# Optimization experiments

Hardware: AMD Instinct MI355X
Metric: run time of the kernel (lower is better)

Reference implementation:

```python
import jax, jax.numpy as jnp
import numpy as np

S = 80.0          # feature_size
LAMBDA_COORD = 5.0
LAMBDA_NOOBJ = 0.5


def setup_inputs() -> dict:
    key = jax.random.key(0)
    k1, k2, k3 = jax.random.split(key, 3)
    pred_tensor = jax.random.uniform(k1, (1024, 80, 80, 5), dtype=jnp.float32)
    target_boxes = jax.random.uniform(k2, (1024, 80, 80, 4), dtype=jnp.float32)
    obj_mask = jax.random.randint(k3, (1024, 80, 80), 0, 2, dtype=jnp.int32)
    return {"pred_tensor": pred_tensor, "target_boxes": target_boxes, "obj_mask": obj_mask}


def _xyxy(w, h):
    # Faithful to the original (buggy) conversion: pred_xyxy[:, :2] = pred[:, 2]/S - 0.5*pred[:, 2:4]
    # i.e. the 'center' used for BOTH x and y is w/S.
    c = w / S
    return c - 0.5 * w, c - 0.5 * h, c + 0.5 * w, c + 0.5 * h


def reference(pred_tensor, target_boxes, obj_mask):
    # pred_tensor: [N, 80, 80, 5]  (x, y, w, h, conf), target_boxes: [N, 80, 80, 4]
    m = (obj_mask > 0).astype(pred_tensor.dtype)        # coord_mask; (1-m) is noobj_mask
    px, py, pw, ph, pc = (pred_tensor[..., i] for i in range(5))
    tx, ty, tw, th = (target_boxes[..., i] for i in range(4))

    # per-cell 1x1 IoU (B=1, so the response-assignment loop is trivial: mask always 1)
    px1, py1, px2, py2 = _xyxy(pw, ph)
    tx1, ty1, tx2, ty2 = _xyxy(tw, th)
    iw = jnp.maximum(jnp.minimum(px2, tx2) - jnp.maximum(px1, tx1), 0.0)
    ih = jnp.maximum(jnp.minimum(py2, ty2) - jnp.maximum(py1, ty1), 0.0)
    inter = iw * ih
    union = pw * ph + tw * th - inter
    iou = jax.lax.stop_gradient(inter / union)          # original uses max_iou.data (detached)

    loss_xy = jnp.sum(m * ((px - tx) ** 2 + (py - ty) ** 2))
    loss_wh = jnp.sum(m * ((jnp.sqrt(pw) - jnp.sqrt(tw)) ** 2 + (jnp.sqrt(ph) - jnp.sqrt(th)) ** 2))
    loss_obj = jnp.sum(m * (pc - iou) ** 2)
    loss_noobj = jnp.sum((1.0 - m) * pc ** 2)           # noobj target conf is 0

    batch = pred_tensor.shape[0]
    loss = (LAMBDA_COORD * (loss_xy + loss_wh) + loss_obj + LAMBDA_NOOBJ * loss_noobj) / batch
    return loss
```

## Files before the change

### kernel.cpp

```cpp
#include <hip/hip_runtime.h>


#define S_INV (1.0f / 80.0f)

__global__ void zero_out_kernel(float* out) {
    out[0] = 0.0f;
}

__global__ __launch_bounds__(256) void yolo_loss_kernel(
    const float4* __restrict__ pred4,
    const float4* __restrict__ targ4,
    const int4*  __restrict__ mask4,
    float* __restrict__ out,
    int ngroups)
{
    __shared__ float4 lp[5 * 256];
    __shared__ float4 lt[5 * 256];

    const int t = threadIdx.x;
    float acc = 0.0f;

    for (int base = blockIdx.x * 256; base < ngroups; base += gridDim.x * 256) {
        #pragma unroll
        for (int i = 0; i < 5; ++i)
            lp[i * 256 + t] = pred4[base * 5 + i * 256 + t];
        #pragma unroll
        for (int i = 0; i < 4; ++i) {
            int j = i * 256 + t;
            lt[j + (j >> 2)] = targ4[base * 4 + j];
        }
        int4 mi = mask4[base + t];
        int mm[4] = { mi.x, mi.y, mi.z, mi.w };
        __syncthreads();

        float p[20];
        float tv[16];
        #pragma unroll
        for (int i = 0; i < 5; ++i) {
            float4 v = lp[5 * t + i];
            p[4 * i + 0] = v.x; p[4 * i + 1] = v.y; p[4 * i + 2] = v.z; p[4 * i + 3] = v.w;
        }
        #pragma unroll
        for (int i = 0; i < 4; ++i) {
            float4 v = lt[5 * t + i];
            tv[4 * i + 0] = v.x; tv[4 * i + 1] = v.y; tv[4 * i + 2] = v.z; tv[4 * i + 3] = v.w;
        }

        #pragma unroll
        for (int j = 0; j < 4; ++j) {
            float px = p[5 * j + 0], py = p[5 * j + 1], pw = p[5 * j + 2];
            float ph = p[5 * j + 3], pc = p[5 * j + 4];
            float tx = tv[4 * j + 0], ty = tv[4 * j + 1], tw = tv[4 * j + 2], th = tv[4 * j + 3];

            float cp = pw * S_INV;
            float ct = tw * S_INV;
            float px1 = cp - 0.5f * pw, py1 = cp - 0.5f * ph;
            float px2 = cp + 0.5f * pw, py2 = cp + 0.5f * ph;
            float tx1 = ct - 0.5f * tw, ty1 = ct - 0.5f * th;
            float tx2 = ct + 0.5f * tw, ty2 = ct + 0.5f * th;

            float iw = fmaxf(fminf(px2, tx2) - fmaxf(px1, tx1), 0.0f);
            float ih = fmaxf(fminf(py2, ty2) - fmaxf(py1, ty1), 0.0f);
            float inter = iw * ih;
            float uni = pw * ph + tw * th - inter;
            float iou = inter / uni;

            float dx = px - tx, dy = py - ty;
            float sw = sqrtf(pw) - sqrtf(tw);
            float sh = sqrtf(ph) - sqrtf(th);
            float dobj = pc - iou;

            float obj_term = 5.0f * ((dx * dx + dy * dy) + (sw * sw + sh * sh)) + dobj * dobj;
            float noobj_term = 0.5f * pc * pc;
            acc += (mm[j] > 0) ? obj_term : noobj_term;
        }
        __syncthreads();
    }

    #pragma unroll
    for (int off = 32; off > 0; off >>= 1)
        acc += __shfl_down(acc, off, 64);

    __shared__ float wsum[4];
    int lane = threadIdx.x & 63;
    int wid = threadIdx.x >> 6;
    if (lane == 0) wsum[wid] = acc;
    __syncthreads();

    if (threadIdx.x == 0) {
        float b = wsum[0] + wsum[1] + wsum[2] + wsum[3];
        atomicAdd(out, b * (1.0f / 1024.0f));
    }
}

extern "C" void kernel_launch(void* const* d_in, const int* in_sizes, int n_in,
                              void* d_out, int out_size, void* d_ws, size_t ws_size,
                              hipStream_t stream) {
    const float4* pred4 = (const float4*)d_in[0];
    const float4* targ4 = (const float4*)d_in[1];
    const int4*   mask4 = (const int4*)d_in[2];
    float* out = (float*)d_out;

    int ncells = in_sizes[2];
    int ngroups = ncells / 4;

    zero_out_kernel<<<1, 1, 0, stream>>>(out);

    const int block = 256;
    const int grid = 2048;
    yolo_loss_kernel<<<grid, block, 0, stream>>>(pred4, targ4, mask4, out, ngroups);
}
```

Before: 56.30 us.

## Double-buffer pred tiles in LDS and prefetch next tile during compute

The pred tile now goes into a double-buffered shared-memory ring. Each iteration issues global loads for the next tile while computing on the current one, so the loop needs one barrier instead of two. Targets and masks are read directly from global memory into registers, since each thread's 4 target boxes are contiguous, which removes the target LDS staging. Pred loads use nontemporal hints, and the block reduction is replaced by one atomic per wavefront. The costs are more register pressure from the prefetched values and four times as many atomics. The tile count assumes the cell count divides evenly into 1024-cell tiles and that the grid does not exceed the tile count.

New measurement: 128.9 us. 2.29x slower.

```diff
diff --git a/kernel.cpp b/kernel.cpp
--- a/kernel.cpp
+++ b/kernel.cpp
@@ -1,112 +1,142 @@
 #include <hip/hip_runtime.h>
+#include <stdint.h>
 
 
 #define S_INV (1.0f / 80.0f)
 
-__global__ void zero_out_kernel(float* out) {
-    out[0] = 0.0f;
+typedef float f4 __attribute__((ext_vector_type(4)));
+typedef int   i4 __attribute__((ext_vector_type(4)));
+
+#define TILE 256
+
+__global__ void zero_out_kernel(float* out) { out[0] = 0.0f; }
+
+struct TM { f4 t0, t1, t2, t3; i4 m; };
+
+__device__ __forceinline__ void load_tm(TM& tm, const f4* __restrict__ targ4,
+                                        const i4* __restrict__ mask4, int gid) {
+    tm.t0 = targ4[4 * gid + 0];
+    tm.t1 = targ4[4 * gid + 1];
+    tm.t2 = targ4[4 * gid + 2];
+    tm.t3 = targ4[4 * gid + 3];
+    tm.m  = mask4[gid];
+}
+
+__device__ __forceinline__ float cell_loss(float px, float py, float pw, float ph, float pc,
+                                           float tx, float ty, float tw, float th, int m)
+{
+    float cp = pw * S_INV;
+    float ct = tw * S_INV;
+    float px1 = cp - 0.5f * pw, py1 = cp - 0.5f * ph;
+    float px2 = cp + 0.5f * pw, py2 = cp + 0.5f * ph;
+    float tx1 = ct - 0.5f * tw, ty1 = ct - 0.5f * th;
+    float tx2 = ct + 0.5f * tw, ty2 = ct + 0.5f * th;
+
+    float iw = fmaxf(fminf(px2, tx2) - fmaxf(px1, tx1), 0.0f);
+    float ih = fmaxf(fminf(py2, ty2) - fmaxf(py1, ty1), 0.0f);
+    float inter = iw * ih;
+    float uni = pw * ph + tw * th - inter;
+    float iou = inter / uni;
+
+    float dx = px - tx, dy = py - ty;
+    float sw = sqrtf(pw) - sqrtf(tw);
+    float sh = sqrtf(ph) - sqrtf(th);
+    float dobj = pc - iou;
+
+    float obj_term = 5.0f * ((dx * dx + dy * dy) + (sw * sw + sh * sh)) + dobj * dobj;
+    float noobj_term = 0.5f * pc * pc;
+    return (m > 0) ? obj_term : noobj_term;
+}
+
+__device__ __forceinline__ float compute_tile(const f4* __restrict__ lbuf, const TM& tm, int t)
+{
+    f4 p0 = lbuf[5 * t + 0], p1 = lbuf[5 * t + 1], p2 = lbuf[5 * t + 2];
+    f4 p3 = lbuf[5 * t + 3], p4 = lbuf[5 * t + 4];
+    float s = 0.0f;
+    s += cell_loss(p0.x, p0.y, p0.z, p0.w, p1.x,
+                   tm.t0.x, tm.t0.y, tm.t0.z, tm.t0.w, tm.m.x);
+    s += cell_loss(p1.y, p1.z, p1.w, p2.x, p2.y,
+                   tm.t1.x, tm.t1.y, tm.t1.z, tm.t1.w, tm.m.y);
+    s += cell_loss(p2.z, p2.w, p3.x, p3.y, p3.z,
+                   tm.t2.x, tm.t2.y, tm.t2.z, tm.t2.w, tm.m.z);
+    s += cell_loss(p3.w, p4.x, p4.y, p4.z, p4.w,
+                   tm.t3.x, tm.t3.y, tm.t3.z, tm.t3.w, tm.m.w);
+    return s;
 }
 
 __global__ __launch_bounds__(256) void yolo_loss_kernel(
-    const float4* __restrict__ pred4,
-    const float4* __restrict__ targ4,
-    const int4*  __restrict__ mask4,
+    const f4* __restrict__ pred4,
+    const f4* __restrict__ targ4,
+    const i4* __restrict__ mask4,
     float* __restrict__ out,
-    int ngroups)
+    int ntiles)
 {
-    __shared__ float4 lp[5 * 256];
-    __shared__ float4 lt[5 * 256];
+    __shared__ f4 buf[2][5 * TILE];
 
-    const int t = threadIdx.x;
+    const int t  = threadIdx.x;
+    const int bid = blockIdx.x;
+    const int nb  = gridDim.x;
     float acc = 0.0f;
 
-    for (int base = blockIdx.x * 256; base < ngroups; base += gridDim.x * 256) {
+    const int cnt = (ntiles - 1 - bid) / nb + 1;
+
+    {
+        const f4* ps = pred4 + (size_t)bid * 5 * TILE;
+        f4 P[5];
         #pragma unroll
         for (int i = 0; i < 5; ++i)
-            lp[i * 256 + t] = pred4[base * 5 + i * 256 + t];
+            P[i] = __builtin_nontemporal_load(ps + i * TILE + t);
         #pragma unroll
-        for (int i = 0; i < 4; ++i) {
-            int j = i * 256 + t;
-            lt[j + (j >> 2)] = targ4[base * 4 + j];
-        }
-        int4 mi = mask4[base + t];
-        int mm[4] = { mi.x, mi.y, mi.z, mi.w };
-        __syncthreads();
+        for (int i = 0; i < 5; ++i)
+            buf[0][i * TILE + t] = P[i];
+    }
+    TM T;
+    load_tm(T, targ4, mask4, bid * TILE + t);
+    __syncthreads();
 
-        float p[20];
-        float tv[16];
+    int cur = 0;
+    for (int j = 1; j < cnt; ++j) {
+        const int tile = bid + j * nb;
+        const f4* ps = pred4 + (size_t)tile * 5 * TILE;
+        f4 P[5];
         #pragma unroll
-        for (int i = 0; i < 5; ++i) {
-            float4 v = lp[5 * t + i];
-            p[4 * i + 0] = v.x; p[4 * i + 1] = v.y; p[4 * i + 2] = v.z; p[4 * i + 3] = v.w;
-        }
-        #pragma unroll
-        for (int i = 0; i < 4; ++i) {
-            float4 v = lt[5 * t + i];
-            tv[4 * i + 0] = v.x; tv[4 * i + 1] = v.y; tv[4 * i + 2] = v.z; tv[4 * i + 3] = v.w;
-        }
+        for (int i = 0; i < 5; ++i)
+            P[i] = __builtin_nontemporal_load(ps + i * TILE + t);
+        TM T2;
+        load_tm(T2, targ4, mask4, tile * TILE + t);
+
+        acc += compute_tile(&buf[cur][0], T, t);
 
         #pragma unroll
-        for (int j = 0; j < 4; ++j) {
-            float px = p[5 * j + 0], py = p[5 * j + 1], pw = p[5 * j + 2];
-            float ph = p[5 * j + 3], pc = p[5 * j + 4];
-            float tx = tv[4 * j + 0], ty = tv[4 * j + 1], tw = tv[4 * j + 2], th = tv[4 * j + 3];
-
-            float cp = pw * S_INV;
-            float ct = tw * S_INV;
-            float px1 = cp - 0.5f * pw, py1 = cp - 0.5f * ph;
-            float px2 = cp + 0.5f * pw, py2 = cp + 0.5f * ph;
-            float tx1 = ct - 0.5f * tw, ty1 = ct - 0.5f * th;
-            float tx2 = ct + 0.5f * tw, ty2 = ct + 0.5f * th;
-
-            float iw = fmaxf(fminf(px2, tx2) - fmaxf(px1, tx1), 0.0f);
-            float ih = fmaxf(fminf(py2, ty2) - fmaxf(py1, ty1), 0.0f);
-            float inter = iw * ih;
-            float uni = pw * ph + tw * th - inter;
-            float iou = inter / uni;
-
-            float dx = px - tx, dy = py - ty;
-            float sw = sqrtf(pw) - sqrtf(tw);
-            float sh = sqrtf(ph) - sqrtf(th);
-            float dobj = pc - iou;
-
-            float obj_term = 5.0f * ((dx * dx + dy * dy) + (sw * sw + sh * sh)) + dobj * dobj;
-            float noobj_term = 0.5f * pc * pc;
-            acc += (mm[j] > 0) ? obj_term : noobj_term;
-        }
+        for (int i = 0; i < 5; ++i)
+            buf[cur ^ 1][i * TILE + t] = P[i];
         __syncthreads();
+        cur ^= 1;
+        T = T2;
     }
+    acc += compute_tile(&buf[cur][0], T, t);
 
     #pragma unroll
     for (int off = 32; off > 0; off >>= 1)
         acc += __shfl_down(acc, off, 64);
-
-    __shared__ float wsum[4];
-    int lane = threadIdx.x & 63;
-    int wid = threadIdx.x >> 6;
-    if (lane == 0) wsum[wid] = acc;
-    __syncthreads();
-
-    if (threadIdx.x == 0) {
-        float b = wsum[0] + wsum[1] + wsum[2] + wsum[3];
-        atomicAdd(out, b * (1.0f / 1024.0f));
-    }
+    if ((t & 63) == 0)
+        atomicAdd(out, acc * (1.0f / 1024.0f));
 }
 
 extern "C" void kernel_launch(void* const* d_in, const int* in_sizes, int n_in,
                               void* d_out, int out_size, void* d_ws, size_t ws_size,
                               hipStream_t stream) {
-    const float4* pred4 = (const float4*)d_in[0];
-    const float4* targ4 = (const float4*)d_in[1];
-    const int4*   mask4 = (const int4*)d_in[2];
+    const f4* pred4 = (const f4*)d_in[0];
+    const f4* targ4 = (const f4*)d_in[1];
+    const i4* mask4 = (const i4*)d_in[2];
     float* out = (float*)d_out;
 
     int ncells = in_sizes[2];
-    int ngroups = ncells / 4;
+    int ntiles = ncells / (4 * TILE);
 
     zero_out_kernel<<<1, 1, 0, stream>>>(out);
 
     const int block = 256;
     const int grid = 2048;
-    yolo_loss_kernel<<<grid, block, 0, stream>>>(pred4, targ4, mask4, out, ngroups);
+    yolo_loss_kernel<<<grid, block, 0, stream>>>(pred4, targ4, mask4, out, ntiles);
 }
```
